# Kernel optimization log

Measured on AMD Instinct MI355X. Metric: run time of the kernel, lower is better.

The kernel has to match this reference:

```python
import jax, jax.numpy as jnp
import numpy as np

EPSILON = 0.1
ALPHA = 0.5
N_ITER = 10
N_USERS = 100000


def setup_inputs() -> dict:
    key = jax.random.key(0)
    k1, k2, k3, k4, k5, k6 = jax.random.split(key, 6)
    B, C, F = 2048, 1024, 128
    users = jax.random.randint(k1, (B,), 0, N_USERS)
    items = jax.random.randint(k2, (B, C), 0, C)
    D = jax.random.uniform(k3, (B, C), minval=0.1, maxval=1.0)
    capacities = jax.random.uniform(k4, (C,), minval=0.5, maxval=1.5)
    # ScaledEmbedding: normal init scaled down by embedding_dim
    item_emb = jax.random.normal(k5, (C, F), dtype=jnp.float32) / F
    user_emb = jax.random.normal(k6, (N_USERS, F), dtype=jnp.float32) / F
    return dict(users=users, items=items, D=D, capacities=capacities,
                item_emb=item_emb, user_emb=user_emb)


def reference(users, items, D, capacities, item_emb, user_emb):
    B, C = D.shape
    ie = item_emb[items]            # [B, C, F] gathered candidate embeddings
    ue = user_emb[users]            # [B, F]
    dot = jnp.einsum('bcf,bf->bc', ie, ue)          # batched dot products
    affinity = (1.0 - ALPHA) * dot - ALPHA * (D / jnp.mean(D))
    K = jnp.exp(affinity / EPSILON)                 # [B, C]

    scaling = B / N_USERS
    a = jnp.ones((B,), K.dtype)
    b = capacities * scaling                        # [C]

    def step(carry, _):
        _, v = carry
        u = a / (K @ v)                             # [B]
        v_new = b / (K.T @ u)                       # [C]
        return (u, v_new), None

    (u, v), _ = jax.lax.scan(step, (a, jnp.ones((C,), K.dtype)),
                             None, length=N_ITER)
    P = K * (u[:, None] * v[None, :])               # K * outer(u, v)
    return P
```

## Files before the change

kernel.cpp:

```cpp
#include <hip/hip_runtime.h>
#include <hip/hip_fp16.h>

#define BB      2048
#define CC      1024
#define FF      128
#define NBLK    256
#define RPB     8
#define TPB     512
#define NITER   10
#define SUBR    8
#define SCALING_F (2048.0f / 100000.0f)

#define NLEAF   8
#define LPB     32
#define NSLOT   (NITER + 1)
#define CPAD    16

__device__ unsigned g_epoch;
__device__ unsigned g_leaf[NSLOT * NLEAF * CPAD];
__device__ unsigned g_root[NSLOT * CPAD];
__device__ unsigned g_rel [NSLOT * CPAD];
__device__ float g_meanPart[NBLK];
__device__ float g_colsum[NITER * SUBR * CC];

__device__ __forceinline__ float atomLoadF(const float* p) {
    return __hip_atomic_load(p, __ATOMIC_RELAXED, __HIP_MEMORY_SCOPE_AGENT);
}
__device__ __forceinline__ void atomStoreF(float* p, float v) {
    __hip_atomic_store(p, v, __ATOMIC_RELAXED, __HIP_MEMORY_SCOPE_AGENT);
}
__device__ __forceinline__ unsigned atomAddU(unsigned* p) {
    return __hip_atomic_fetch_add(p, 1u, __ATOMIC_RELAXED,
                                  __HIP_MEMORY_SCOPE_AGENT);
}

__device__ __forceinline__ void tree_barrier(int slot, unsigned e,
                                             int bid, int tid) {
    __syncthreads();
    if (tid == 0) {
        const int leaf = bid >> 5;
        unsigned rl = atomAddU(&g_leaf[(slot * NLEAF + leaf) * CPAD]);
        if (rl == e * LPB + (LPB - 1)) {
            unsigned rr = atomAddU(&g_root[slot * CPAD]);
            if (rr == e * NLEAF + (NLEAF - 1))
                __hip_atomic_store(&g_rel[slot * CPAD], e + 1u,
                                   __ATOMIC_RELAXED, __HIP_MEMORY_SCOPE_AGENT);
        }
        while ((int)(__hip_atomic_load(&g_rel[slot * CPAD], __ATOMIC_RELAXED,
                                       __HIP_MEMORY_SCOPE_AGENT) - (e + 1u)) < 0)
            ;
    }
    __syncthreads();
}

__global__ void __launch_bounds__(TPB)
fused_sinkhorn(const int* __restrict__ users, const int* __restrict__ items,
               const float* __restrict__ D, const float* __restrict__ caps,
               const float* __restrict__ iemb, const float* __restrict__ uemb,
               float* __restrict__ out) {
    const int bid = blockIdx.x, tid = threadIdx.x;
    const int r0 = bid * RPB;

    __shared__ union { float ue[RPB][FF]; float v[CC]; } uv;
    __shared__ __half dott[RPB][CC];
    __shared__ float  Kt[RPB][CC];
    __shared__ float  ush[RPB];
    __shared__ float  red[TPB / 64];
    __shared__ float  s2sh;
    __shared__ unsigned s_epoch;

    if (tid == 0) s_epoch = atomAddU(&g_epoch) >> 8;

    const float4* Dg  = (const float4*)(D + ((size_t)r0 << 10));
    const int4*   it4 = (const int4*)(items + ((size_t)r0 << 10));
    float4 d_reg[4];
    int4   it_reg[4];
    #pragma unroll
    for (int k = 0; k < 4; ++k) d_reg[k]  = Dg[tid + k * TPB];
    #pragma unroll
    for (int k = 0; k < 4; ++k) it_reg[k] = it4[tid + k * TPB];

    const float cap0 = caps[tid]       * SCALING_F;
    const float cap1 = caps[tid + 512] * SCALING_F;

    for (int i = bid * TPB + tid; i < NITER * SUBR * CC; i += NBLK * TPB)
        atomStoreF(&g_colsum[i], 0.0f);

    if (tid < 256) {
        int r = tid >> 5, f4 = tid & 31;
        int u = users[r0 + r];
        ((float4*)uv.ue[r])[f4] = ((const float4*)(uemb + (size_t)u * FF))[f4];
    }

    float p = 0.0f;
    #pragma unroll
    for (int k = 0; k < 4; ++k) {
        float4 d = d_reg[k];
        p += d.x + d.y + d.z + d.w;
    }
    #pragma unroll
    for (int off = 32; off > 0; off >>= 1) p += __shfl_down(p, off, 64);
    if ((tid & 63) == 0) red[tid >> 6] = p;
    __syncthreads();
    const unsigned e = s_epoch;
    if (tid == 0) {
        float s = 0.0f;
        #pragma unroll
        for (int k = 0; k < TPB / 64; ++k) s += red[k];
        atomStoreF(&g_meanPart[bid], s);
    }

    {
        const float4* us  = (const float4*)uv.ue;
        const float4* ip0 = (const float4*)(iemb + (size_t)tid * FF);
        const float4* ip1 = (const float4*)(iemb + (size_t)(tid + 512) * FF);
        float acc0[RPB] = {}, acc1[RPB] = {};
        for (int f4 = 0; f4 < FF / 4; ++f4) {
            float4 a0 = ip0[f4], a1 = ip1[f4];
            #pragma unroll
            for (int r = 0; r < RPB; ++r) {
                float4 b = us[r * (FF / 4) + f4];
                acc0[r] += a0.x * b.x + a0.y * b.y + a0.z * b.z + a0.w * b.w;
                acc1[r] += a1.x * b.x + a1.y * b.y + a1.z * b.z + a1.w * b.w;
            }
        }
        #pragma unroll
        for (int r = 0; r < RPB; ++r) {
            dott[r][tid]       = __float2half(acc0[r]);
            dott[r][tid + 512] = __float2half(acc1[r]);
        }
    }

    tree_barrier(NITER, e, bid, tid);

    if (tid < 64) {
        float s = 0.0f;
        #pragma unroll
        for (int k = 0; k < NBLK / 64; ++k)
            s += atomLoadF(&g_meanPart[tid + 64 * k]);
        #pragma unroll
        for (int off = 32; off > 0; off >>= 1) s += __shfl_down(s, off, 64);
        if (tid == 0) s2sh = 5.0f * (float)(BB * CC) / s;
    }
    __syncthreads();
    const float s2 = s2sh;
    float4* KtL = (float4*)Kt;
    #pragma unroll
    for (int k = 0; k < 4; ++k) {
        int    i  = tid + k * TPB;
        int4   iv = it_reg[k];
        float4 d  = d_reg[k];
        int    r  = i >> 8;
        float4 kv;
        kv.x = __expf(5.0f * __half2float(dott[r][iv.x]) - s2 * d.x);
        kv.y = __expf(5.0f * __half2float(dott[r][iv.y]) - s2 * d.y);
        kv.z = __expf(5.0f * __half2float(dott[r][iv.z]) - s2 * d.z);
        kv.w = __expf(5.0f * __half2float(dott[r][iv.w]) - s2 * d.w);
        KtL[i] = kv;
    }

    for (int t = 0; t < NITER; ++t) {
        if (t == 0) {
            uv.v[tid]       = 1.0f;
            uv.v[tid + 512] = 1.0f;
        } else {
            const float* base = g_colsum + (size_t)(t - 1) * SUBR * CC;
            float t0[SUBR], t1[SUBR];
            #pragma unroll
            for (int k = 0; k < SUBR; ++k) t0[k] = atomLoadF(&base[k * CC + tid]);
            #pragma unroll
            for (int k = 0; k < SUBR; ++k) t1[k] = atomLoadF(&base[k * CC + tid + 512]);
            float s0 = 0.0f, s1 = 0.0f;
            #pragma unroll
            for (int k = 0; k < SUBR; ++k) { s0 += t0[k]; s1 += t1[k]; }
            uv.v[tid]       = cap0 / s0;
            uv.v[tid + 512] = cap1 / s1;
        }
        __syncthreads();

        {
            int r = tid >> 6, l = tid & 63;
            const float4* kr = (const float4*)Kt[r];
            const float4* v4 = (const float4*)uv.v;
            float pp = 0.0f;
            #pragma unroll
            for (int i2 = 0; i2 < 4; ++i2) {
                float4 k = kr[l + i2 * 64], v = v4[l + i2 * 64];
                pp += k.x * v.x + k.y * v.y + k.z * v.z + k.w * v.w;
            }
            #pragma unroll
            for (int off = 32; off > 0; off >>= 1) pp += __shfl_down(pp, off, 64);
            if (l == 0) ush[r] = 1.0f / pp;
        }
        __syncthreads();

        {
            float* cb = g_colsum + ((size_t)t * SUBR + (bid & (SUBR - 1))) * CC;
            float sA = 0.0f, sB = 0.0f;
            #pragma unroll
            for (int r = 0; r < RPB; ++r) {
                sA += Kt[r][tid]       * ush[r];
                sB += Kt[r][tid + 512] * ush[r];
            }
            atomicAdd(&cb[tid],       sA);
            atomicAdd(&cb[tid + 512], sB);
        }

        tree_barrier(t, e, bid, tid);
    }

    {
        const float* base = g_colsum + (size_t)(NITER - 1) * SUBR * CC;
        float t0[SUBR], t1[SUBR];
        #pragma unroll
        for (int k = 0; k < SUBR; ++k) t0[k] = atomLoadF(&base[k * CC + tid]);
        #pragma unroll
        for (int k = 0; k < SUBR; ++k) t1[k] = atomLoadF(&base[k * CC + tid + 512]);
        float s0 = 0.0f, s1 = 0.0f;
        #pragma unroll
        for (int k = 0; k < SUBR; ++k) { s0 += t0[k]; s1 += t1[k]; }
        uv.v[tid]       = cap0 / s0;
        uv.v[tid + 512] = cap1 / s1;
    }
    __syncthreads();

    float4* o4 = (float4*)(out + ((size_t)r0 << 10));
    #pragma unroll
    for (int k = 0; k < 4; ++k) {
        int    i  = tid + k * TPB;
        int    r  = i >> 8;
        float4 kk = KtL[i];
        float  ur = ush[r];
        float4 v  = *(const float4*)&uv.v[(i * 4) & (CC - 1)];
        float4 pv;
        pv.x = kk.x * ur * v.x;  pv.y = kk.y * ur * v.y;
        pv.z = kk.z * ur * v.z;  pv.w = kk.w * ur * v.w;
        o4[i] = pv;
    }
}

extern "C" void kernel_launch(void* const* d_in, const int* in_sizes, int n_in,
                              void* d_out, int out_size, void* d_ws, size_t ws_size,
                              hipStream_t stream) {
    const int*   users = (const int*)d_in[0];
    const int*   items = (const int*)d_in[1];
    const float* D     = (const float*)d_in[2];
    const float* caps  = (const float*)d_in[3];
    const float* iemb  = (const float*)d_in[4];
    const float* uemb  = (const float*)d_in[5];
    float* out = (float*)d_out;

    hipLaunchKernelGGL(fused_sinkhorn, dim3(NBLK), dim3(TPB), 0, stream,
                       users, items, D, caps, iemb, uemb, out);
}
```

Baseline: 182.5 us.

## Redistribute Sinkhorn iterations onto 64 blocks with K staged through global memory

All 256 blocks still compute K for 8 rows each and write it to a global scratch buffer. After a barrier, only 64 blocks continue, each loading 32 rows of K (128KB) into shared memory to run the 10 Sinkhorn iterations and write the output. This shrinks the per-iteration grid barrier from 256 to 64 participants and cuts the colsum atomic traffic, at the cost of an extra global round-trip of K and less parallelism in the iteration phase. The shared-memory dot buffer is unioned with the larger K tile to make room.

New measurement: 193.7 us. +6.1%, slower.

```diff
diff --git a/kernel.cpp b/kernel.cpp
--- a/kernel.cpp
+++ b/kernel.cpp
@@ -9,19 +9,21 @@
 #define TPB     512
 #define NITER   10
 #define SUBR    8
+#define NIB     64
+#define RPIB    32
 #define SCALING_F (2048.0f / 100000.0f)
-
-#define NLEAF   8
-#define LPB     32
-#define NSLOT   (NITER + 1)
 #define CPAD    16
 
 __device__ unsigned g_epoch;
-__device__ unsigned g_leaf[NSLOT * NLEAF * CPAD];
-__device__ unsigned g_root[NSLOT * CPAD];
-__device__ unsigned g_rel [NSLOT * CPAD];
+__device__ unsigned g_leafA[2 * 8 * CPAD];
+__device__ unsigned g_rootA[2 * CPAD];
+__device__ unsigned g_relA [2 * CPAD];
+__device__ unsigned g_leafB[NITER * 8 * CPAD];
+__device__ unsigned g_rootB[NITER * CPAD];
+__device__ unsigned g_relB [NITER * CPAD];
 __device__ float g_meanPart[NBLK];
 __device__ float g_colsum[NITER * SUBR * CC];
+__device__ unsigned long long g_K64[BB * CC / 2];
 
 __device__ __forceinline__ float atomLoadF(const float* p) {
     return __hip_atomic_load(p, __ATOMIC_RELAXED, __HIP_MEMORY_SCOPE_AGENT);
@@ -33,24 +35,27 @@
     return __hip_atomic_fetch_add(p, 1u, __ATOMIC_RELAXED,
                                   __HIP_MEMORY_SCOPE_AGENT);
 }
-
-__device__ __forceinline__ void tree_barrier(int slot, unsigned e,
-                                             int bid, int tid) {
-    __syncthreads();
-    if (tid == 0) {
-        const int leaf = bid >> 5;
-        unsigned rl = atomAddU(&g_leaf[(slot * NLEAF + leaf) * CPAD]);
-        if (rl == e * LPB + (LPB - 1)) {
-            unsigned rr = atomAddU(&g_root[slot * CPAD]);
-            if (rr == e * NLEAF + (NLEAF - 1))
-                __hip_atomic_store(&g_rel[slot * CPAD], e + 1u,
-                                   __ATOMIC_RELAXED, __HIP_MEMORY_SCOPE_AGENT);
-        }
-        while ((int)(__hip_atomic_load(&g_rel[slot * CPAD], __ATOMIC_RELAXED,
-                                       __HIP_MEMORY_SCOPE_AGENT) - (e + 1u)) < 0)
-            ;
-    }
-    __syncthreads();
+__device__ __forceinline__ unsigned loadU(const unsigned* p) {
+    return __hip_atomic_load(p, __ATOMIC_RELAXED, __HIP_MEMORY_SCOPE_AGENT);
+}
+__device__ __forceinline__ void storeU(unsigned* p, unsigned v) {
+    __hip_atomic_store(p, v, __ATOMIC_RELAXED, __HIP_MEMORY_SCOPE_AGENT);
+}
+__device__ __forceinline__ unsigned long long
+atomLoadU64(const unsigned long long* p) {
+    return __hip_atomic_load(p, __ATOMIC_RELAXED, __HIP_MEMORY_SCOPE_AGENT);
+}
+__device__ __forceinline__ void
+atomStoreU64(unsigned long long* p, unsigned long long v) {
+    __hip_atomic_store(p, v, __ATOMIC_RELAXED, __HIP_MEMORY_SCOPE_AGENT);
+}
+__device__ __forceinline__ unsigned long long packF2(float a, float b) {
+    union { float f[2]; unsigned long long u; } x;
+    x.f[0] = a; x.f[1] = b; return x.u;
+}
+__device__ __forceinline__ float2 unpackF2(unsigned long long u) {
+    union { float f[2]; unsigned long long u; } x;
+    x.u = u; return make_float2(x.f[0], x.f[1]);
 }
 
 __global__ void __launch_bounds__(TPB)
@@ -61,10 +66,12 @@
     const int bid = blockIdx.x, tid = threadIdx.x;
     const int r0 = bid * RPB;
 
-    __shared__ union { float ue[RPB][FF]; float v[CC]; } uv;
-    __shared__ __half dott[RPB][CC];
-    __shared__ float  Kt[RPB][CC];
-    __shared__ float  ush[RPB];
+    __shared__ __align__(16) union {
+        __half dott[RPB][CC];
+        float  Kt[RPIB * CC];
+    } kk;
+    __shared__ __align__(16) union { float ue[RPB][FF]; float v[CC]; } uv;
+    __shared__ float  ush[RPIB];
     __shared__ float  red[TPB / 64];
     __shared__ float  s2sh;
     __shared__ unsigned s_epoch;
@@ -126,12 +133,21 @@
         }
         #pragma unroll
         for (int r = 0; r < RPB; ++r) {
-            dott[r][tid]       = __float2half(acc0[r]);
-            dott[r][tid + 512] = __float2half(acc1[r]);
-        }
-    }
-
-    tree_barrier(NITER, e, bid, tid);
+            kk.dott[r][tid]       = __float2half(acc0[r]);
+            kk.dott[r][tid + 512] = __float2half(acc1[r]);
+        }
+    }
+
+    __syncthreads();
+    if (tid == 0) {
+        unsigned rl = atomAddU(&g_leafA[(0 * 8 + (bid >> 5)) * CPAD]);
+        if (rl == e * 32 + 31) {
+            unsigned rr = atomAddU(&g_rootA[0 * CPAD]);
+            if (rr == e * 8 + 7) storeU(&g_relA[0 * CPAD], e + 1u);
+        }
+        while ((int)(loadU(&g_relA[0 * CPAD]) - (e + 1u)) < 0) ;
+    }
+    __syncthreads();
 
     if (tid < 64) {
         float s = 0.0f;
@@ -144,20 +160,52 @@
     }
     __syncthreads();
     const float s2 = s2sh;
-    float4* KtL = (float4*)Kt;
-    #pragma unroll
-    for (int k = 0; k < 4; ++k) {
-        int    i  = tid + k * TPB;
-        int4   iv = it_reg[k];
-        float4 d  = d_reg[k];
-        int    r  = i >> 8;
-        float4 kv;
-        kv.x = __expf(5.0f * __half2float(dott[r][iv.x]) - s2 * d.x);
-        kv.y = __expf(5.0f * __half2float(dott[r][iv.y]) - s2 * d.y);
-        kv.z = __expf(5.0f * __half2float(dott[r][iv.z]) - s2 * d.z);
-        kv.w = __expf(5.0f * __half2float(dott[r][iv.w]) - s2 * d.w);
-        KtL[i] = kv;
-    }
+    {
+        unsigned long long* dst64 = g_K64 + (size_t)bid * (RPB * CC / 2);
+        #pragma unroll
+        for (int k = 0; k < 4; ++k) {
+            int    i  = tid + k * TPB;
+            int4   iv = it_reg[k];
+            float4 d  = d_reg[k];
+            int    r  = i >> 8;
+            float kx = __expf(5.0f * __half2float(kk.dott[r][iv.x]) - s2 * d.x);
+            float ky = __expf(5.0f * __half2float(kk.dott[r][iv.y]) - s2 * d.y);
+            float kz = __expf(5.0f * __half2float(kk.dott[r][iv.z]) - s2 * d.z);
+            float kw = __expf(5.0f * __half2float(kk.dott[r][iv.w]) - s2 * d.w);
+            atomStoreU64(&dst64[2 * i],     packF2(kx, ky));
+            atomStoreU64(&dst64[2 * i + 1], packF2(kz, kw));
+        }
+    }
+
+    __syncthreads();
+    if (tid == 0) {
+        unsigned rl = atomAddU(&g_leafA[(1 * 8 + (bid >> 5)) * CPAD]);
+        if (rl == e * 32 + 31) {
+            unsigned rr = atomAddU(&g_rootA[1 * CPAD]);
+            if (rr == e * 8 + 7) storeU(&g_relA[1 * CPAD], e + 1u);
+        }
+    }
+    if (bid >= NIB) return;
+    if (tid == 0)
+        while ((int)(loadU(&g_relA[1 * CPAD]) - (e + 1u)) < 0) ;
+    __syncthreads();
+
+    {
+        const unsigned long long* src64 = g_K64 + (size_t)bid * (RPIB * CC / 2);
+        float2* kt2 = (float2*)kk.Kt;
+        for (int m = 0; m < 32; m += 8) {
+            unsigned long long tmp[8];
+            #pragma unroll
+            for (int q = 0; q < 8; ++q)
+                tmp[q] = atomLoadU64(&src64[tid + (m + q) * TPB]);
+            #pragma unroll
+            for (int q = 0; q < 8; ++q)
+                kt2[tid + (m + q) * TPB] = unpackF2(tmp[q]);
+        }
+    }
+    __syncthreads();
+    const float*  Ktf = kk.Kt;
+    const float4* Kt4 = (const float4*)kk.Kt;
 
     for (int t = 0; t < NITER; ++t) {
         if (t == 0) {
@@ -179,18 +227,23 @@
         __syncthreads();
 
         {
-            int r = tid >> 6, l = tid & 63;
-            const float4* kr = (const float4*)Kt[r];
+            int w = tid >> 6, l = tid & 63;
             const float4* v4 = (const float4*)uv.v;
-            float pp = 0.0f;
-            #pragma unroll
-            for (int i2 = 0; i2 < 4; ++i2) {
-                float4 k = kr[l + i2 * 64], v = v4[l + i2 * 64];
-                pp += k.x * v.x + k.y * v.y + k.z * v.z + k.w * v.w;
+            #pragma unroll
+            for (int rr = 0; rr < 4; ++rr) {
+                int row = (w << 2) + rr;
+                const float4* kr = Kt4 + row * (CC / 4);
+                float pp = 0.0f;
+                #pragma unroll
+                for (int i2 = 0; i2 < 4; ++i2) {
+                    float4 k = kr[l + i2 * 64], v = v4[l + i2 * 64];
+                    pp += k.x * v.x + k.y * v.y + k.z * v.z + k.w * v.w;
+                }
+                #pragma unroll
+                for (int off = 32; off > 0; off >>= 1)
+                    pp += __shfl_down(pp, off, 64);
+                if (l == 0) ush[row] = 1.0f / pp;
             }
-            #pragma unroll
-            for (int off = 32; off > 0; off >>= 1) pp += __shfl_down(pp, off, 64);
-            if (l == 0) ush[r] = 1.0f / pp;
         }
         __syncthreads();
 
@@ -198,15 +251,25 @@
             float* cb = g_colsum + ((size_t)t * SUBR + (bid & (SUBR - 1))) * CC;
             float sA = 0.0f, sB = 0.0f;
             #pragma unroll
-            for (int r = 0; r < RPB; ++r) {
-                sA += Kt[r][tid]       * ush[r];
-                sB += Kt[r][tid + 512] * ush[r];
+            for (int r = 0; r < RPIB; ++r) {
+                float u = ush[r];
+                sA += Ktf[r * CC + tid]       * u;
+                sB += Ktf[r * CC + tid + 512] * u;
             }
             atomicAdd(&cb[tid],       sA);
             atomicAdd(&cb[tid + 512], sB);
         }
 
-        tree_barrier(t, e, bid, tid);
+        __syncthreads();
+        if (tid == 0) {
+            unsigned rl = atomAddU(&g_leafB[(t * 8 + (bid >> 3)) * CPAD]);
+            if (rl == e * 8 + 7) {
+                unsigned rr = atomAddU(&g_rootB[t * CPAD]);
+                if (rr == e * 8 + 7) storeU(&g_relB[t * CPAD], e + 1u);
+            }
+            while ((int)(loadU(&g_relB[t * CPAD]) - (e + 1u)) < 0) ;
+        }
+        __syncthreads();
     }
 
     {
@@ -224,17 +287,17 @@
     }
     __syncthreads();
 
-    float4* o4 = (float4*)(out + ((size_t)r0 << 10));
-    #pragma unroll
-    for (int k = 0; k < 4; ++k) {
-        int    i  = tid + k * TPB;
-        int    r  = i >> 8;
-        float4 kk = KtL[i];
-        float  ur = ush[r];
-        float4 v  = *(const float4*)&uv.v[(i * 4) & (CC - 1)];
+    float4* o4 = (float4*)out + (size_t)bid * (RPIB * CC / 4);
+    #pragma unroll
+    for (int c = 0; c < 16; ++c) {
+        int    i   = tid + c * TPB;
+        int    row = i >> 8;
+        float4 kv  = Kt4[i];
+        float  ur  = ush[row];
+        float4 v   = ((const float4*)uv.v)[i & 255];
         float4 pv;
-        pv.x = kk.x * ur * v.x;  pv.y = kk.y * ur * v.y;
-        pv.z = kk.z * ur * v.z;  pv.w = kk.w * ur * v.w;
+        pv.x = kv.x * ur * v.x;  pv.y = kv.y * ur * v.y;
+        pv.z = kv.z * ur * v.z;  pv.w = kv.w * ur * v.w;
         o4[i] = pv;
     }
 }
```
